# Kernel tuning notes

Hardware: AMD Instinct MI355X
Metric: run time of the kernel (lower is better)

Reference implementation:

```python
import jax, jax.numpy as jnp
import numpy as np

N_HEAD = 32
N_KV = 8
HEAD_DIM = 64  # n_embd // n_head = 2048 // 32
EPS = 1e-6


def bit_linear(x, w):
    """BitNet b1.58 BitLinear (no bias): int8 absmax activation quant (per-token),
    ternary mean-absmax weight quant, straight-through estimator."""
    s = 127.0 / jnp.clip(jnp.max(jnp.abs(x), axis=-1, keepdims=True), 1e-5)
    xq = jnp.clip(jnp.round(x * s), -128.0, 127.0) / s
    xq = x + jax.lax.stop_gradient(xq - x)
    ws = 1.0 / jnp.clip(jnp.mean(jnp.abs(w)), 1e-5)
    wq = jnp.clip(jnp.round(w * ws), -1.0, 1.0) / ws
    wq = w + jax.lax.stop_gradient(wq - w)
    return xq @ wq.T


def sub_ln(x, gamma, beta):
    mean = jnp.mean(x, axis=-1, keepdims=True)
    var = jnp.mean((x - mean) ** 2, axis=-1, keepdims=True)
    return (x - mean) / jnp.sqrt(var + EPS) * gamma + beta


def setup_inputs() -> dict:
    key = jax.random.key(0)
    ks = jax.random.split(key, 8)
    D, KV, F = 2048, 512, 8192
    B, T = 1, 2048
    w_scale = 0.02
    return {
        "x": jax.random.normal(ks[0], (B, T, D), jnp.float32),
        "g1": jnp.ones((D,), jnp.float32),
        "b1": jnp.zeros((D,), jnp.float32),
        "g2": jnp.ones((D,), jnp.float32),
        "b2": jnp.zeros((D,), jnp.float32),
        "wq": jax.random.normal(ks[1], (D, D), jnp.float32) * w_scale,
        "wk": jax.random.normal(ks[2], (KV, D), jnp.float32) * w_scale,
        "wv": jax.random.normal(ks[3], (KV, D), jnp.float32) * w_scale,
        "wo": jax.random.normal(ks[4], (D, D), jnp.float32) * w_scale,
        "w1": jax.random.normal(ks[5], (F, D), jnp.float32) * w_scale,
        "w2": jax.random.normal(ks[6], (D, F), jnp.float32) * w_scale,
    }


def reference(x, g1, b1, g2, b2, wq, wk, wv, wo, w1, w2):
    B, T, D = x.shape
    # --- attention sublayer (pre-norm, residual) ---
    h = sub_ln(x, g1, b1)
    q = bit_linear(h, wq).reshape(B, T, N_HEAD, HEAD_DIM)
    k = bit_linear(h, wk).reshape(B, T, N_KV, HEAD_DIM)
    v = bit_linear(h, wv).reshape(B, T, N_KV, HEAD_DIM)
    rep = N_HEAD // N_KV
    k = jnp.repeat(k, rep, axis=2)  # GQA repeat_interleave
    v = jnp.repeat(v, rep, axis=2)
    attn = jnp.einsum('bqhd,bkhd->bhqk', q, k) * (HEAD_DIM ** -0.5)
    causal = jnp.tril(jnp.ones((T, T), bool))
    attn = jnp.where(causal, attn, -jnp.inf)
    attn = jax.nn.softmax(attn, axis=-1)
    o = jnp.einsum('bhqk,bkhd->bqhd', attn, v).reshape(B, T, D)
    x = x + bit_linear(o, wo)
    # --- FFN sublayer (pre-norm, residual, ReLU^2) ---
    h2 = sub_ln(x, g2, b2)
    f = bit_linear(h2, w1)
    f = jnp.maximum(f, 0.0) ** 2
    return x + bit_linear(f, w2)
```

## Files before the change

### kernel.cpp

```cpp
#include <hip/hip_runtime.h>
#include <hip/hip_bf16.h>
#include <stdint.h>

typedef __bf16 bf16;
typedef signed char i8;
typedef __bf16 v8bf __attribute__((ext_vector_type(8)));
typedef __bf16 v4bf __attribute__((ext_vector_type(4)));
typedef signed char v8i8 __attribute__((ext_vector_type(8)));
typedef int    v4i  __attribute__((ext_vector_type(4)));
typedef float  f32x16 __attribute__((ext_vector_type(16)));

#define MFMA32(a,b,c)   __builtin_amdgcn_mfma_f32_32x32x16_bf16((a),(b),(c),0,0,0)
#define MFMA_I8(a,b,c)  __builtin_amdgcn_mfma_i32_16x16x64_i8((a),(b),(c),0,0,0)

__device__ __forceinline__ void glds16(const void* g, void* l) {
  __builtin_amdgcn_global_load_lds(
      (const __attribute__((address_space(1))) void*)g,
      (__attribute__((address_space(3))) void*)l, 16, 0, 0);
}

__device__ __forceinline__ float wred_sum(float v) {
#pragma unroll
  for (int o = 32; o; o >>= 1) v += __shfl_xor(v, o);
  return v;
}
__device__ __forceinline__ float wred_max(float v) {
#pragma unroll
  for (int o = 32; o; o >>= 1) v = fmaxf(v, __shfl_xor(v, o));
  return v;
}

__device__ __forceinline__ unsigned int packbf(float a, float b) {
  union { bf16 h[2]; unsigned int u; } x;
  x.h[0] = (bf16)a; x.h[1] = (bf16)b;
  return x.u;
}

__global__ void k_sniff(const unsigned short* __restrict__ x, int* __restrict__ flag) {
  int cnt = 0;
  for (int i = threadIdx.x; i < 2048; i += 64) {
    const unsigned short u = x[i];
    const int e = (u >> 7) & 0xFF;
    if (u == 0 || (e >= 100 && e <= 140)) cnt++;
  }
#pragma unroll
  for (int o = 32; o; o >>= 1) cnt += __shfl_xor(cnt, o);
  if (threadIdx.x == 0) flag[0] = (cnt >= 1844) ? 0 : 1;
}


__global__ void k_zero(float* p, int n) {
  int i = threadIdx.x;
  if (i < n) p[i] = 0.0f;
}

__global__ __launch_bounds__(256) void k_zerof(float4* __restrict__ p) {
  p[(size_t)blockIdx.x * 256 + threadIdx.x] = make_float4(0.f, 0.f, 0.f, 0.f);
}

__global__ __launch_bounds__(256) void k_abssum(const void* __restrict__ w, int n,
                                                const int* __restrict__ flag,
                                                float* __restrict__ out) {
  const int tid = threadIdx.x;
  const int f32 = flag[0];
  __shared__ float sred[4];
  float s = 0.0f;
  if (f32) {
    const float4* p = (const float4*)w;
    for (int i = (blockIdx.x * 256 + tid) * 2; i * 4 < n; i += gridDim.x * 512) {
      float4 a = p[i], b = p[i + 1];
      s += fabsf(a.x) + fabsf(a.y) + fabsf(a.z) + fabsf(a.w) +
           fabsf(b.x) + fabsf(b.y) + fabsf(b.z) + fabsf(b.w);
    }
  } else {
    const bf16* p = (const bf16*)w;
    for (int i = (blockIdx.x * 256 + tid) * 8; i < n; i += gridDim.x * 2048) {
      v8bf v = *(const v8bf*)(p + i);
#pragma unroll
      for (int j = 0; j < 8; j++) s += fabsf((float)v[j]);
    }
  }
  s = wred_sum(s);
  if ((tid & 63) == 0) sred[tid >> 6] = s;
  __syncthreads();
  if (tid == 0) atomicAdd(out, sred[0] + sred[1] + sred[2] + sred[3]);
}

__global__ __launch_bounds__(256) void k_wquant(const void* __restrict__ w, i8* __restrict__ o,
                                                const float* __restrict__ sum, float invn,
                                                const int* __restrict__ flag) {
  const int gid = blockIdx.x * 256 + threadIdx.x;
  const int i = gid * 8;
  const float ws = 1.0f / fmaxf(sum[0] * invn, 1e-5f);
  const int f32 = flag[0];
  float v[8];
  if (f32) {
    float4 a = ((const float4*)w)[gid * 2];
    float4 b = ((const float4*)w)[gid * 2 + 1];
    v[0] = a.x; v[1] = a.y; v[2] = a.z; v[3] = a.w;
    v[4] = b.x; v[5] = b.y; v[6] = b.z; v[7] = b.w;
  } else {
    v8bf t = *(const v8bf*)((const bf16*)w + i);
#pragma unroll
    for (int j = 0; j < 8; j++) v[j] = (float)t[j];
  }
  v8i8 r;
#pragma unroll
  for (int j = 0; j < 8; j++) {
    float t = rintf(v[j] * ws);
    r[j] = (i8)fminf(fmaxf(t, -1.0f), 1.0f);
  }
  *(v8i8*)(o + i) = r;
}

template <bool XINT>
__global__ __launch_bounds__(256) void k_lnq(const void* __restrict__ x, const void* __restrict__ g,
                                             const void* __restrict__ b, i8* __restrict__ q,
                                             float* __restrict__ sc, const int* __restrict__ flag) {
  const int row = blockIdx.x, tid = threadIdx.x;
  const int f32 = flag[0];
  __shared__ float sred[4];
  float v[8];
#pragma unroll
  for (int i = 0; i < 8; i++) {
    const size_t idx = (size_t)row * 2048 + tid + 256 * i;
    if (XINT)      v[i] = ((const float*)x)[idx];
    else if (f32)  v[i] = ((const float*)x)[idx];
    else           v[i] = (float)((const bf16*)x)[idx];
  }
  float s = 0.0f;
#pragma unroll
  for (int i = 0; i < 8; i++) s += v[i];
  s = wred_sum(s);
  if ((tid & 63) == 0) sred[tid >> 6] = s;
  __syncthreads();
  const float mean = (sred[0] + sred[1] + sred[2] + sred[3]) * (1.0f / 2048.0f);
  __syncthreads();
  float vs = 0.0f;
#pragma unroll
  for (int i = 0; i < 8; i++) { float d = v[i] - mean; vs += d * d; }
  vs = wred_sum(vs);
  if ((tid & 63) == 0) sred[tid >> 6] = vs;
  __syncthreads();
  const float rstd = rsqrtf((sred[0] + sred[1] + sred[2] + sred[3]) * (1.0f / 2048.0f) + 1e-6f);
  __syncthreads();
  float hq[8];
  float am = 0.0f;
#pragma unroll
  for (int i = 0; i < 8; i++) {
    const int c = tid + 256 * i;
    const float gv = f32 ? ((const float*)g)[c] : (float)((const bf16*)g)[c];
    const float bv = f32 ? ((const float*)b)[c] : (float)((const bf16*)b)[c];
    hq[i] = (v[i] - mean) * rstd * gv + bv;
    am = fmaxf(am, fabsf(hq[i]));
  }
  am = wred_max(am);
  if ((tid & 63) == 0) sred[tid >> 6] = am;
  __syncthreads();
  am = fmaxf(fmaxf(sred[0], sred[1]), fmaxf(sred[2], sred[3]));
  const float cl = fmaxf(am, 1e-5f);
  const float s127 = 127.0f / cl;
#pragma unroll
  for (int i = 0; i < 8; i++) {
    float r = rintf(hq[i] * s127);
    r = fminf(fmaxf(r, -128.0f), 127.0f);
    q[(size_t)row * 2048 + tid + 256 * i] = (i8)r;
  }
  if (tid == 0) sc[row] = cl * (1.0f / 127.0f);
}

template <int IT>
__global__ __launch_bounds__(256) void k_rowq(const bf16* __restrict__ in, i8* __restrict__ q,
                                              float* __restrict__ sc) {
  const int row = blockIdx.x, tid = threadIdx.x;
  const int C = IT * 256;
  __shared__ float sred[4];
  const bf16* xr = in + (size_t)row * C;
  float v[IT];
  float am = 0.0f;
#pragma unroll
  for (int i = 0; i < IT; i++) {
    v[i] = (float)xr[tid + 256 * i];
    am = fmaxf(am, fabsf(v[i]));
  }
  am = wred_max(am);
  if ((tid & 63) == 0) sred[tid >> 6] = am;
  __syncthreads();
  am = fmaxf(fmaxf(sred[0], sred[1]), fmaxf(sred[2], sred[3]));
  const float cl = fmaxf(am, 1e-5f);
  const float s127 = 127.0f / cl;
#pragma unroll
  for (int i = 0; i < IT; i++) {
    float r = rintf(v[i] * s127);
    r = fminf(fmaxf(r, -128.0f), 127.0f);
    q[(size_t)row * C + tid + 256 * i] = (i8)r;
  }
  if (tid == 0) sc[row] = cl * (1.0f / 127.0f);
}

template <int EPI>
__global__ __launch_bounds__(256) void k_gemm(const i8* __restrict__ A, const i8* __restrict__ B,
                                              const float* __restrict__ sA,
                                              const float* __restrict__ wsum, float winv,
                                              void* __restrict__ out,
                                              int M, int N, int K, int Kc,
                                              const int* __restrict__ flag) {
  __shared__ __align__(16) i8 As[128 * 64];
  __shared__ __align__(16) i8 Bs[128 * 64];
  const int tid = threadIdx.x;
  const int lane = tid & 63;
  const int ml = lane & 15;
  const int q4 = lane >> 4;
  const int wid = tid >> 6;
  const int wM = wid >> 1;
  const int wN = wid & 1;
  const int m0 = blockIdx.y * 128;
  const int n0 = blockIdx.x * 128;

  const int r0 = tid >> 2;
  const int c0 = (tid & 3) * 16;
  const i8* Ag0 = A + (size_t)(m0 + r0) * K + c0;
  const i8* Ag1 = Ag0 + (size_t)64 * K;
  const i8* Bg0 = B + (size_t)(n0 + r0) * K + c0;
  const i8* Bg1 = Bg0 + (size_t)64 * K;
  i8* as0 = &As[wid * 1024];
  i8* as1 = &As[4096 + wid * 1024];
  i8* bs0 = &Bs[wid * 1024];
  i8* bs1 = &Bs[4096 + wid * 1024];

  v4i acc[4][4] = {};

  const int kbeg = blockIdx.z * Kc;
  const int kfin = kbeg + Kc;
  for (int k0 = kbeg; k0 < kfin; k0 += 64) {
    __syncthreads();
    glds16(Ag0 + k0, as0);
    glds16(Ag1 + k0, as1);
    glds16(Bg0 + k0, bs0);
    glds16(Bg1 + k0, bs1);
    __syncthreads();
    v4i af[4], bfr[4];
#pragma unroll
    for (int i = 0; i < 4; i++) af[i] = *(const v4i*)&As[(wM * 64 + i * 16 + ml) * 64 + q4 * 16];
#pragma unroll
    for (int j = 0; j < 4; j++) bfr[j] = *(const v4i*)&Bs[(wN * 64 + j * 16 + ml) * 64 + q4 * 16];
#pragma unroll
    for (int i = 0; i < 4; i++)
#pragma unroll
      for (int j = 0; j < 4; j++) acc[i][j] = MFMA_I8(af[i], bfr[j], acc[i][j]);
  }

  if (EPI == 4) {
    int* ob = (int*)out;
#pragma unroll
    for (int i = 0; i < 4; i++)
#pragma unroll
      for (int r = 0; r < 4; r++) {
        const int row = m0 + wM * 64 + i * 16 + q4 * 4 + r;
#pragma unroll
        for (int j = 0; j < 4; j++) {
          const int col = n0 + wN * 64 + j * 16 + ml;
          atomicAdd(ob + (size_t)row * N + col, acc[i][j][r]);
        }
      }
    return;
  }

  const float cw = fmaxf(wsum[0] * winv, 1e-5f);
#pragma unroll
  for (int i = 0; i < 4; i++) {
#pragma unroll
    for (int r = 0; r < 4; r++) {
      const int row = m0 + wM * 64 + i * 16 + q4 * 4 + r;
      const float sa = sA[row] * cw;
#pragma unroll
      for (int j = 0; j < 4; j++) {
        const int col = n0 + wN * 64 + j * 16 + ml;
        const float val = (float)acc[i][j][r] * sa;
        float u = fmaxf(val, 0.0f);
        ((bf16*)out)[(size_t)row * N + col] = (bf16)(u * u);
      }
    }
  }
}

template <int MODE>
__global__ __launch_bounds__(256) void k_epi(const int* __restrict__ acc, int lda, int cofs,
                                             int ncols,
                                             const float* __restrict__ sA,
                                             const float* __restrict__ wsum, float winv,
                                             const void* __restrict__ resid,
                                             void* __restrict__ out,
                                             const int* __restrict__ flag) {
  const int row = blockIdx.x, tid = threadIdx.x;
  const float cw = fmaxf(wsum[0] * winv, 1e-5f);
  const float srow = (MODE == 3) ? cw : sA[row] * cw;
  const int f32 = flag[0];
  for (int c = tid * 4; c < ncols; c += 1024) {
    const v4i a = *(const v4i*)(acc + (size_t)row * lda + cofs + c);
    float s0 = srow, s1 = srow, s2 = srow, s3 = srow;
    if (MODE == 3) {
      float4 sc = *(const float4*)(sA + c);
      s0 *= sc.x; s1 *= sc.y; s2 *= sc.z; s3 *= sc.w;
    }
    const float v0 = (float)a[0] * s0, v1 = (float)a[1] * s1;
    const float v2 = (float)a[2] * s2, v3 = (float)a[3] * s3;
    const size_t o = (size_t)row * ncols + c;
    if (MODE == 0 || MODE == 3) {
      v4bf r;
      r[0] = (bf16)v0; r[1] = (bf16)v1; r[2] = (bf16)v2; r[3] = (bf16)v3;
      *(v4bf*)((bf16*)out + o) = r;
    } else if (MODE == 1) {
      float4 rv;
      if (f32) {
        rv = *(const float4*)((const float*)resid + o);
      } else {
        const v4bf rb = *(const v4bf*)((const bf16*)resid + o);
        rv = make_float4((float)rb[0], (float)rb[1], (float)rb[2], (float)rb[3]);
      }
      *(float4*)((float*)out + o) = make_float4(rv.x + v0, rv.y + v1, rv.z + v2, rv.w + v3);
    } else {
      const float4 rv = *(const float4*)((const float*)resid + o);
      const float o0 = rv.x + v0, o1 = rv.y + v1, o2 = rv.z + v2, o3 = rv.w + v3;
      if (f32) {
        *(float4*)((float*)out + o) = make_float4(o0, o1, o2, o3);
      } else {
        v4bf r;
        r[0] = (bf16)o0; r[1] = (bf16)o1; r[2] = (bf16)o2; r[3] = (bf16)o3;
        *(v4bf*)((bf16*)out + o) = r;
      }
    }
  }
}

__global__ __launch_bounds__(64) void k_attn(const bf16* __restrict__ Q, const bf16* __restrict__ Kb,
                                             const bf16* __restrict__ Vt, bf16* __restrict__ O) {
  const int h = blockIdx.y;
  const int kvh = h >> 2;
  const int t = (blockIdx.x + ((h >> 2) << 3)) & 63;
  const int qw0 = t * 32;
  const int lane = threadIdx.x;
  const int ql = lane & 31;
  const int hi = lane >> 5;

  v8bf qf[4];
  {
    const bf16* qp = Q + (size_t)(qw0 + ql) * 2048 + h * 64 + hi * 8;
#pragma unroll
    for (int c = 0; c < 4; c++) qf[c] = *(const v8bf*)(qp + c * 16);
  }

  float m = -1e30f, l = 0.0f;
  f32x16 acc0 = {}, acc1 = {};

  const bf16* kbase = Kb + kvh * 64 + hi * 8;
  const bf16* vbase = Vt + (size_t)(kvh * 64 + ql) * 2048 + hi * 8;

  for (int kb = 0; kb <= qw0; kb += 32) {
    f32x16 s = {};
    {
      const bf16* kp = kbase + (size_t)(kb + ql) * 512;
#pragma unroll
      for (int c = 0; c < 4; c++) {
        const v8bf kf = *(const v8bf*)(kp + c * 16);
        s = MFMA32(kf, qf[c], s);
      }
    }
    const bool diag = (kb == qw0);
    float p[16];
    float rm = -1e30f;
#pragma unroll
    for (int r = 0; r < 16; r++) {
      float v = s[r] * 0.125f;
      const int koff = (r & 3) + ((r >> 2) << 3) + (hi << 2);
      if (diag && koff > ql) v = -1e30f;
      p[r] = v;
      rm = fmaxf(rm, v);
    }
    rm = fmaxf(rm, __shfl_xor(rm, 32));
    const float mn = fmaxf(m, rm);
    const float alpha = __expf(m - mn);
    m = mn;
    float rs = 0.0f;
#pragma unroll
    for (int r = 0; r < 16; r++) {
      p[r] = __expf(p[r] - mn);
      rs += p[r];
    }
    rs += __shfl_xor(rs, 32);
    l = l * alpha + rs;
#pragma unroll
    for (int r = 0; r < 16; r++) { acc0[r] *= alpha; acc1[r] *= alpha; }

    unsigned int w0 = packbf(p[0], p[1]),   w2 = packbf(p[4], p[5]);
    unsigned int w1 = packbf(p[2], p[3]),   w3 = packbf(p[6], p[7]);
    unsigned int x0 = packbf(p[8], p[9]),   x2 = packbf(p[12], p[13]);
    unsigned int x1 = packbf(p[10], p[11]), x3 = packbf(p[14], p[15]);
    asm("v_permlane32_swap_b32 %0, %1" : "+v"(w0), "+v"(w2));
    asm("v_permlane32_swap_b32 %0, %1" : "+v"(w1), "+v"(w3));
    asm("v_permlane32_swap_b32 %0, %1" : "+v"(x0), "+v"(x2));
    asm("v_permlane32_swap_b32 %0, %1" : "+v"(x1), "+v"(x3));
    union BU { unsigned int u[4]; v8bf v; } B0, B1;
    B0.u[0] = w0; B0.u[1] = w1; B0.u[2] = w2; B0.u[3] = w3;
    B1.u[0] = x0; B1.u[1] = x1; B1.u[2] = x2; B1.u[3] = x3;

    const bf16* vp = vbase + kb;
    const v8bf v00 = *(const v8bf*)(vp);
    const v8bf v01 = *(const v8bf*)(vp + 16);
    const v8bf v10 = *(const v8bf*)(vp + (size_t)32 * 2048);
    const v8bf v11 = *(const v8bf*)(vp + (size_t)32 * 2048 + 16);
    acc0 = MFMA32(v00, B0.v, acc0);
    acc0 = MFMA32(v01, B1.v, acc0);
    acc1 = MFMA32(v10, B0.v, acc1);
    acc1 = MFMA32(v11, B1.v, acc1);
  }

  const float inv = 1.0f / l;
  unsigned int* op = (unsigned int*)(O + (size_t)(qw0 + ql) * 2048 + h * 64);
#pragma unroll
  for (int r = 0; r < 16; r += 2) {
    const int d = (r & 3) + ((r >> 2) << 3) + (hi << 2);
    op[d >> 1] = packbf(acc0[r] * inv, acc0[r + 1] * inv);
    op[(d >> 1) + 16] = packbf(acc1[r] * inv, acc1[r + 1] * inv);
  }
}

extern "C" void kernel_launch(void* const* d_in, const int* in_sizes, int n_in, void* d_out,
                              int out_size, void* d_ws, size_t ws_size, hipStream_t stream) {
  const void* x = d_in[0];
  const void* g1 = d_in[1];
  const void* b1 = d_in[2];
  const void* g2 = d_in[3];
  const void* b2 = d_in[4];
  const void* wq = d_in[5];
  const void* wk = d_in[6];
  const void* wv = d_in[7];
  const void* wo = d_in[8];
  const void* w1 = d_in[9];
  const void* w2 = d_in[10];

  char* ws = (char*)d_ws;
  const size_t MB = 1ull << 20;
  float* wsum = (float*)ws;
  float* s1 = (float*)(ws + 8192);
  float* so = (float*)(ws + 16384);
  float* s2 = (float*)(ws + 24576);
  float* sf = (float*)(ws + 32768);
  int* flag = (int*)(ws + 40960);
  char* big = ws + 65536;

  i8* w1z = (i8*)(big);
  i8* fq  = (i8*)(big);
  i8* w2z = (i8*)(big + 16 * MB);
  i8* wqz = (i8*)(big + 32 * MB);
  i8* wkz = (i8*)(big + 36 * MB);
  i8* wvz = (i8*)(big + 37 * MB);
  i8* woz = (i8*)(big + 38 * MB);
  i8* xq1 = (i8*)(big + 42 * MB);
  i8* oq  = xq1;
  i8* xq2 = xq1;
  int* accQK = (int*)(big + 46 * MB);
  int* accO  = (int*)(big + 46 * MB);
  bf16* Fb   = (bf16*)(big + 46 * MB);
  int* accF  = (int*)(big + 46 * MB);
  int* accVt = (int*)(big + 66 * MB);
  bf16* Qb   = (bf16*)(big + 70 * MB);
  bf16* Kbuf = (bf16*)(big + 78 * MB);
  bf16* Vt   = (bf16*)(big + 80 * MB);
  bf16* Ob   = (bf16*)(big + 82 * MB);
  float* x1  = (float*)(big + 78 * MB);

  const float invD2 = 1.0f / 4194304.0f;
  const float invKV = 1.0f / 1048576.0f;
  const float invF = 1.0f / 16777216.0f;

  k_sniff<<<1, 64, 0, stream>>>((const unsigned short*)x, flag);
  k_zero<<<1, 64, 0, stream>>>(wsum, 8);
  k_zerof<<<6144, 256, 0, stream>>>((float4*)accQK);

  k_abssum<<<512, 256, 0, stream>>>(wq, 2048 * 2048, flag, wsum + 0);
  k_abssum<<<512, 256, 0, stream>>>(wk, 512 * 2048, flag, wsum + 1);
  k_abssum<<<512, 256, 0, stream>>>(wv, 512 * 2048, flag, wsum + 2);
  k_abssum<<<512, 256, 0, stream>>>(wo, 2048 * 2048, flag, wsum + 3);
  k_abssum<<<512, 256, 0, stream>>>(w1, 8192 * 2048, flag, wsum + 4);
  k_abssum<<<512, 256, 0, stream>>>(w2, 2048 * 8192, flag, wsum + 5);
  k_wquant<<<2048, 256, 0, stream>>>(wq, wqz, wsum + 0, invD2, flag);
  k_wquant<<<512, 256, 0, stream>>>(wk, wkz, wsum + 1, invKV, flag);
  k_wquant<<<512, 256, 0, stream>>>(wv, wvz, wsum + 2, invKV, flag);
  k_wquant<<<2048, 256, 0, stream>>>(wo, woz, wsum + 3, invD2, flag);
  k_wquant<<<8192, 256, 0, stream>>>(w1, w1z, wsum + 4, invF, flag);
  k_wquant<<<8192, 256, 0, stream>>>(w2, w2z, wsum + 5, invF, flag);

  k_lnq<false><<<2048, 256, 0, stream>>>(x, g1, b1, xq1, s1, flag);
  k_gemm<4><<<dim3(20, 16, 4), 256, 0, stream>>>(xq1, wqz, s1, wsum + 0, invD2, accQK,
                                                 2048, 2560, 2048, 512, flag);
  k_gemm<4><<<dim3(16, 4, 4), 256, 0, stream>>>(wvz, xq1, s1, wsum + 2, invKV, accVt,
                                                512, 2048, 2048, 512, flag);
  k_epi<0><<<2048, 256, 0, stream>>>(accQK, 2560, 0, 2048, s1, wsum + 0, invD2, nullptr, Qb, flag);
  k_epi<0><<<2048, 256, 0, stream>>>(accQK, 2560, 2048, 512, s1, wsum + 1, invKV, nullptr, Kbuf, flag);
  k_epi<3><<<512, 256, 0, stream>>>(accVt, 2048, 0, 2048, s1, wsum + 2, invKV, nullptr, Vt, flag);
  k_attn<<<dim3(64, 32), 64, 0, stream>>>(Qb, Kbuf, Vt, Ob);
  k_rowq<8><<<2048, 256, 0, stream>>>(Ob, oq, so);
  k_zerof<<<4096, 256, 0, stream>>>((float4*)accO);
  k_gemm<4><<<dim3(16, 16, 4), 256, 0, stream>>>(oq, woz, so, wsum + 3, invD2, accO,
                                                 2048, 2048, 2048, 512, flag);
  k_epi<1><<<2048, 256, 0, stream>>>(accO, 2048, 0, 2048, so, wsum + 3, invD2, x, x1, flag);

  k_lnq<true><<<2048, 256, 0, stream>>>(x1, g2, b2, xq2, s2, flag);
  k_gemm<2><<<dim3(64, 16, 1), 256, 0, stream>>>(xq2, w1z, s2, wsum + 4, invF, Fb,
                                                 2048, 8192, 2048, 2048, flag);
  k_rowq<32><<<2048, 256, 0, stream>>>(Fb, fq, sf);
  k_zerof<<<4096, 256, 0, stream>>>((float4*)accF);
  k_gemm<4><<<dim3(16, 16, 4), 256, 0, stream>>>(fq, w2z, sf, wsum + 5, invF, accF,
                                                 2048, 2048, 8192, 2048, flag);
  k_epi<2><<<2048, 256, 0, stream>>>(accF, 2048, 0, 2048, sf, wsum + 5, invF, x1, d_out, flag);
}
```

Measured before the change: 715.8 us.

## Split long causal attention rows across three KV chunks and merge partials

The attention kernel now splits the query tiles in the second half of the sequence into three KV-range chunks, each computed by its own block. Partial accumulators and per-row max/sum go to workspace and are combined by a new merge kernel. This balances the causal triangle's uneven per-tile work and raises parallelism. It also adds a lazy rescale that skips the online-softmax correction unless the max grows by more than 8. The cost is an extra kernel launch, extra fp32 traffic for the partials, and reshuffled workspace buffers that could alias incorrectly.

```diff
diff --git a/kernel.cpp b/kernel.cpp
--- a/kernel.cpp
+++ b/kernel.cpp
@@ -334,10 +334,23 @@
 }
 
 __global__ __launch_bounds__(64) void k_attn(const bf16* __restrict__ Q, const bf16* __restrict__ Kb,
-                                             const bf16* __restrict__ Vt, bf16* __restrict__ O) {
+                                             const bf16* __restrict__ Vt, bf16* __restrict__ O,
+                                             float* __restrict__ Pacc, float* __restrict__ Ml) {
   const int h = blockIdx.y;
   const int kvh = h >> 2;
-  const int t = (blockIdx.x + ((h >> 2) << 3)) & 63;
+  const int x = blockIdx.x;
+  int t, b0, b1, z;
+  if (x < 32) {
+    t = x; b0 = 0; b1 = t + 1; z = 0;
+  } else {
+    const int e = x - 32;
+    t = 32 + e / 3;
+    z = e - (t - 32) * 3;
+    const int nb = t + 1;
+    b0 = (z * nb) / 3;
+    b1 = ((z + 1) * nb) / 3;
+  }
+  if (t >= 64) return;
   const int qw0 = t * 32;
   const int lane = threadIdx.x;
   const int ql = lane & 31;
@@ -356,7 +369,7 @@
   const bf16* kbase = Kb + kvh * 64 + hi * 8;
   const bf16* vbase = Vt + (size_t)(kvh * 64 + ql) * 2048 + hi * 8;
 
-  for (int kb = 0; kb <= qw0; kb += 32) {
+  for (int kb = b0 * 32; kb < b1 * 32; kb += 32) {
     f32x16 s = {};
     {
       const bf16* kp = kbase + (size_t)(kb + ql) * 512;
@@ -378,19 +391,22 @@
       rm = fmaxf(rm, v);
     }
     rm = fmaxf(rm, __shfl_xor(rm, 32));
-    const float mn = fmaxf(m, rm);
-    const float alpha = __expf(m - mn);
-    m = mn;
+    if (!__all(rm <= m + 8.0f)) {
+      const float mn = fmaxf(m, rm);
+      const float alpha = __expf(m - mn);
+      l *= alpha;
+#pragma unroll
+      for (int r = 0; r < 16; r++) { acc0[r] *= alpha; acc1[r] *= alpha; }
+      m = mn;
+    }
     float rs = 0.0f;
 #pragma unroll
     for (int r = 0; r < 16; r++) {
-      p[r] = __expf(p[r] - mn);
+      p[r] = __expf(p[r] - m);
       rs += p[r];
     }
     rs += __shfl_xor(rs, 32);
-    l = l * alpha + rs;
-#pragma unroll
-    for (int r = 0; r < 16; r++) { acc0[r] *= alpha; acc1[r] *= alpha; }
+    l += rs;
 
     unsigned int w0 = packbf(p[0], p[1]),   w2 = packbf(p[4], p[5]);
     unsigned int w1 = packbf(p[2], p[3]),   w3 = packbf(p[6], p[7]);
@@ -415,14 +431,55 @@
     acc1 = MFMA32(v11, B1.v, acc1);
   }
 
-  const float inv = 1.0f / l;
-  unsigned int* op = (unsigned int*)(O + (size_t)(qw0 + ql) * 2048 + h * 64);
-#pragma unroll
-  for (int r = 0; r < 16; r += 2) {
-    const int d = (r & 3) + ((r >> 2) << 3) + (hi << 2);
-    op[d >> 1] = packbf(acc0[r] * inv, acc0[r + 1] * inv);
-    op[(d >> 1) + 16] = packbf(acc1[r] * inv, acc1[r + 1] * inv);
-  }
+  if (x < 32) {
+    const float inv = 1.0f / l;
+    unsigned int* op = (unsigned int*)(O + (size_t)(qw0 + ql) * 2048 + h * 64);
+#pragma unroll
+    for (int r = 0; r < 16; r += 2) {
+      const int d = (r & 3) + ((r >> 2) << 3) + (hi << 2);
+      op[d >> 1] = packbf(acc0[r] * inv, acc0[r + 1] * inv);
+      op[(d >> 1) + 16] = packbf(acc1[r] * inv, acc1[r + 1] * inv);
+    }
+  } else {
+    float* pb = Pacc + ((size_t)((h * 32 + (t - 32)) * 3 + z)) * 2048 + ql * 64;
+#pragma unroll
+    for (int r = 0; r < 16; r += 2) {
+      const int d = (r & 3) + ((r >> 2) << 3) + (hi << 2);
+      *(float2*)(pb + d) = make_float2(acc0[r], acc0[r + 1]);
+      *(float2*)(pb + 32 + d) = make_float2(acc1[r], acc1[r + 1]);
+    }
+    if (hi == 0) {
+      float* mlp = Ml + ((size_t)((h * 32 + (t - 32)) * 3 + z)) * 64;
+      mlp[ql] = m;
+      mlp[32 + ql] = l;
+    }
+  }
+}
+
+__global__ __launch_bounds__(256) void k_amerge(const float* __restrict__ Pacc,
+                                                const float* __restrict__ Ml,
+                                                bf16* __restrict__ O) {
+  const int tb = blockIdx.x, h = blockIdx.y, tid = threadIdx.x;
+  const int q = tid >> 3;
+  const int d0 = (tid & 7) * 8;
+  const size_t idx = (size_t)(h * 32 + tb) * 3;
+  const float* mlp = Ml + idx * 64;
+  const float m0 = mlp[q],       l0 = mlp[32 + q];
+  const float m1 = mlp[64 + q],  l1 = mlp[96 + q];
+  const float m2 = mlp[128 + q], l2 = mlp[160 + q];
+  const float M = fmaxf(fmaxf(m0, m1), m2);
+  const float w0 = __expf(m0 - M), w1 = __expf(m1 - M), w2 = __expf(m2 - M);
+  const float inv = 1.0f / (w0 * l0 + w1 * l1 + w2 * l2);
+  const float* p = Pacc + idx * 2048 + q * 64 + d0;
+  unsigned int u[4];
+#pragma unroll
+  for (int j = 0; j < 8; j += 2) {
+    const float a = (w0 * p[j] + w1 * p[2048 + j] + w2 * p[4096 + j]) * inv;
+    const float b = (w0 * p[j + 1] + w1 * p[2048 + j + 1] + w2 * p[4096 + j + 1]) * inv;
+    u[j >> 1] = packbf(a, b);
+  }
+  *(uint4*)((char*)O + ((size_t)((32 + tb) * 32 + q) * 2048 + h * 64 + d0) * 2) =
+      make_uint4(u[0], u[1], u[2], u[3]);
 }
 
 extern "C" void kernel_launch(void* const* d_in, const int* in_sizes, int n_in, void* d_out,
@@ -458,17 +515,19 @@
   i8* woz = (i8*)(big + 38 * MB);
   i8* xq1 = (i8*)(big + 42 * MB);
   i8* oq  = xq1;
-  i8* xq2 = xq1;
   int* accQK = (int*)(big + 46 * MB);
+  int* accVt = (int*)(big + 66 * MB);
+  float* Pacc = (float*)(big + 42 * MB);
+  float* Ml   = (float*)(big + 66 * MB);
+  bf16* Kbuf = (bf16*)(big + 70 * MB);
+  bf16* Vt   = (bf16*)(big + 72 * MB);
+  bf16* Qb   = (bf16*)(big + 74 * MB);
+  bf16* Ob   = (bf16*)(big + 82 * MB);
   int* accO  = (int*)(big + 46 * MB);
-  bf16* Fb   = (bf16*)(big + 46 * MB);
-  int* accF  = (int*)(big + 46 * MB);
-  int* accVt = (int*)(big + 66 * MB);
-  bf16* Qb   = (bf16*)(big + 70 * MB);
-  bf16* Kbuf = (bf16*)(big + 78 * MB);
-  bf16* Vt   = (bf16*)(big + 80 * MB);
-  bf16* Ob   = (bf16*)(big + 82 * MB);
-  float* x1  = (float*)(big + 78 * MB);
+  float* x1  = (float*)(big + 80 * MB);
+  i8* xq2 = (i8*)(big + 74 * MB);
+  bf16* Fb   = (bf16*)(big + 42 * MB);
+  int* accF  = (int*)(big + 42 * MB);
 
   const float invD2 = 1.0f / 4194304.0f;
   const float invKV = 1.0f / 1048576.0f;
@@ -499,7 +558,8 @@
   k_epi<0><<<2048, 256, 0, stream>>>(accQK, 2560, 0, 2048, s1, wsum + 0, invD2, nullptr, Qb, flag);
   k_epi<0><<<2048, 256, 0, stream>>>(accQK, 2560, 2048, 512, s1, wsum + 1, invKV, nullptr, Kbuf, flag);
   k_epi<3><<<512, 256, 0, stream>>>(accVt, 2048, 0, 2048, s1, wsum + 2, invKV, nullptr, Vt, flag);
-  k_attn<<<dim3(64, 32), 64, 0, stream>>>(Qb, Kbuf, Vt, Ob);
+  k_attn<<<dim3(128, 32), 64, 0, stream>>>(Qb, Kbuf, Vt, Ob, Pacc, Ml);
+  k_amerge<<<dim3(32, 32), 256, 0, stream>>>(Pacc, Ml, Ob);
   k_rowq<8><<<2048, 256, 0, stream>>>(Ob, oq, so);
   k_zerof<<<4096, 256, 0, stream>>>((float4*)accO);
   k_gemm<4><<<dim3(16, 16, 4), 256, 0, stream>>>(oq, woz, so, wsum + 3, invD2, accO,
```

New measurement: 753.7 us. 5.3% more time.
